# Optimization experiments

Measured on AMD Instinct MI355X. Metric: run time of the kernel, lower is better.

The kernel has to match this reference:

```python
import jax, jax.numpy as jnp
import numpy as np

N_NODES = 50000
N_EDGES = 800000
N_GRAPHS = 64
F_IN = 128
HID = 64
HEADS = 4
N_CLS = 10
NEG_SLOPE = 0.2


def _glorot(key, shape):
    fan_in, fan_out = shape[-1], shape[-2] if len(shape) > 1 else shape[-1]
    lim = jnp.sqrt(6.0 / (fan_in + fan_out))
    return jax.random.uniform(key, shape, jnp.float32, -lim, lim)


def setup_inputs() -> dict:
    key = jax.random.key(0)
    ks = jax.random.split(key, 20)
    x = jax.random.normal(ks[0], (N_NODES, F_IN), jnp.float32)
    edge_index = jax.random.randint(ks[1], (2, N_EDGES), 0, N_NODES, jnp.int32)
    batch = jnp.sort(jax.random.randint(ks[2], (N_NODES,), 0, N_GRAPHS, jnp.int32))
    HC = HID * HEADS
    return {
        "x": x, "edge_index": edge_index, "batch": batch,
        # node embedding Linear(F_IN -> HID)
        "W_emb": _glorot(ks[3], (HID, F_IN)), "b_emb": jnp.zeros((HID,), jnp.float32),
        # gat1: HID -> HID, heads=4, concat
        "W1": _glorot(ks[4], (HC, HID)),
        "a_src1": _glorot(ks[5], (HEADS, HID)), "a_dst1": _glorot(ks[6], (HEADS, HID)),
        "b1": jnp.zeros((HC,), jnp.float32),
        # gat2: HC -> HID, heads=4, concat
        "W2": _glorot(ks[7], (HC, HC)),
        "a_src2": _glorot(ks[8], (HEADS, HID)), "a_dst2": _glorot(ks[9], (HEADS, HID)),
        "b2": jnp.zeros((HC,), jnp.float32),
        # gat3: HC -> HID, heads=1, mean
        "W3": _glorot(ks[10], (HID, HC)),
        "a_src3": _glorot(ks[11], (1, HID)), "a_dst3": _glorot(ks[12], (1, HID)),
        "b3": jnp.zeros((HID,), jnp.float32),
        # classifier: Linear(2*HID -> HID), ReLU, Linear(HID -> N_CLS)
        "Wc1": _glorot(ks[13], (HID, 2 * HID)), "bc1": jnp.zeros((HID,), jnp.float32),
        "Wc2": _glorot(ks[14], (N_CLS, HID)), "bc2": jnp.zeros((N_CLS,), jnp.float32),
    }


def _gat_layer(x, src, dst, W, a_src, a_dst, b, concat):
    """PyG-style GATConv (eval mode, self-loops already in src/dst)."""
    N = x.shape[0]
    H, C = a_src.shape
    h = (x @ W.T).reshape(N, H, C)                       # [N,H,C]
    s = jnp.einsum("nhc,hc->nh", h, a_src)               # [N,H]
    d = jnp.einsum("nhc,hc->nh", h, a_dst)               # [N,H]
    e = jax.nn.leaky_relu(s[src] + d[dst], NEG_SLOPE)    # [E,H]
    emax = jax.lax.stop_gradient(jax.ops.segment_max(e, dst, num_segments=N))
    emax = jnp.where(jnp.isfinite(emax), emax, 0.0)
    ex = jnp.exp(e - emax[dst])
    den = jax.ops.segment_sum(ex, dst, num_segments=N)   # [N,H]
    alpha = ex / (den[dst] + 1e-16)                      # segment softmax
    out = jax.ops.segment_sum(h[src] * alpha[:, :, None], dst, num_segments=N)
    out = out.reshape(N, H * C) if concat else out.mean(axis=1)
    return out + b


def reference(x, edge_index, batch, W_emb, b_emb, W1, a_src1, a_dst1, b1,
              W2, a_src2, a_dst2, b2, W3, a_src3, a_dst3, b3, Wc1, bc1, Wc2, bc2):
    N = x.shape[0]
    loops = jnp.arange(N, dtype=edge_index.dtype)
    src = jnp.concatenate([edge_index[0], loops])
    dst = jnp.concatenate([edge_index[1], loops])

    h = x @ W_emb.T + b_emb
    h = jax.nn.elu(_gat_layer(h, src, dst, W1, a_src1, a_dst1, b1, True))
    h = jax.nn.elu(_gat_layer(h, src, dst, W2, a_src2, a_dst2, b2, True))
    h = jax.nn.elu(_gat_layer(h, src, dst, W3, a_src3, a_dst3, b3, False))

    counts = jax.ops.segment_sum(jnp.ones((N,), h.dtype), batch, num_segments=N_GRAPHS)
    mean = jax.ops.segment_sum(h, batch, num_segments=N_GRAPHS) / jnp.maximum(counts, 1.0)[:, None]
    mx = jax.ops.segment_max(h, batch, num_segments=N_GRAPHS)
    mx = jnp.where(counts[:, None] > 0, mx, 0.0)
    g = jnp.concatenate([mean, mx], axis=1)              # [B, 2*HID]

    g = jax.nn.relu(g @ Wc1.T + bc1)
    return g @ Wc2.T + bc2                               # [B, N_CLS]
```

## Files before the change

kernel.cpp:

```cpp
#include <hip/hip_runtime.h>
#include <math.h>

#define NG 64
#define F_IN 128
#define NEG_SLOPE 0.2f

typedef __attribute__((ext_vector_type(8))) short s16x8;
typedef __attribute__((ext_vector_type(4))) float f32x4;

static __device__ __forceinline__ float elu_f(float x) { return x > 0.f ? x : expm1f(x); }
static __device__ __forceinline__ float lrelu(float x) { return x > 0.f ? x : NEG_SLOPE * x; }
static __device__ __forceinline__ unsigned enc_f32(float x) {
    unsigned u = __float_as_uint(x);
    return (u & 0x80000000u) ? ~u : (u | 0x80000000u);
}
static __device__ __forceinline__ float dec_f32(unsigned u) {
    unsigned b = (u & 0x80000000u) ? (u & 0x7fffffffu) : ~u;
    return __uint_as_float(b);
}
static __device__ __forceinline__ unsigned short bf16_rn(float x) {
    unsigned u = __float_as_uint(x);
    unsigned r = u + 0x7FFFu + ((u >> 16) & 1u);
    return (unsigned short)(r >> 16);
}
static __device__ __forceinline__ float bf16_to_f32(unsigned short h) {
    return __uint_as_float(((unsigned)h) << 16);
}
static __device__ __forceinline__ unsigned pack_split(float x) {
    unsigned short hi = bf16_rn(x);
    unsigned short lo = bf16_rn(x - bf16_to_f32(hi));
    return ((unsigned)hi << 16) | lo;
}

__global__ void convert_pack(const float* __restrict__ in, unsigned* __restrict__ out, int n) {
    int idx = (blockIdx.x * blockDim.x + threadIdx.x) * 4;
    if (idx + 3 < n) {
        float4 v = *(const float4*)&in[idx];
        uint4 o;
        o.x = pack_split(v.x); o.y = pack_split(v.y);
        o.z = pack_split(v.z); o.w = pack_split(v.w);
        *(uint4*)&out[idx] = o;
    }
}

__global__ void uvec_kernel(const float* __restrict__ W1, const float* __restrict__ a1s,
                            const float* __restrict__ a1d,
                            float* __restrict__ us, float* __restrict__ ud) {
    int h = threadIdx.x >> 6;
    int i = threadIdx.x & 63;
    float s = 0.f, d = 0.f;
    for (int o = 0; o < 64; ++o) {
        float w = W1[(h * 64 + o) * 64 + i];
        s = fmaf(w, a1s[h * 64 + o], s);
        d = fmaf(w, a1d[h * 64 + o], d);
    }
    us[h * 64 + i] = s;
    ud[h * 64 + i] = d;
}

__global__ void hist_kernel(const int* __restrict__ ei, int* __restrict__ cnt, int E, int N) {
    int e = blockIdx.x * blockDim.x + threadIdx.x;
    int ET = E + N;
    if (e >= ET) return;
    int dst = (e < E) ? ei[E + e] : (e - E);
    atomicAdd(&cnt[dst], 1);
}

__global__ void scan1_kernel(const int* __restrict__ cnt, int* __restrict__ excl,
                             int* __restrict__ bsum, int n) {
    __shared__ int sm[256];
    int t = threadIdx.x;
    int base = blockIdx.x * 1024 + t * 4;
    int v[4];
    #pragma unroll
    for (int u = 0; u < 4; ++u) { int idx = base + u; v[u] = (idx < n) ? cnt[idx] : 0; }
    int tsum = v[0] + v[1] + v[2] + v[3];
    sm[t] = tsum;
    __syncthreads();
    for (int off = 1; off < 256; off <<= 1) {
        int y = (t >= off) ? sm[t - off] : 0;
        __syncthreads();
        sm[t] += y;
        __syncthreads();
    }
    int run = sm[t] - tsum;
    #pragma unroll
    for (int u = 0; u < 4; ++u) {
        int idx = base + u;
        if (idx < n) excl[idx] = run;
        run += v[u];
    }
    if (t == 255) bsum[blockIdx.x] = sm[255];
}

__global__ void scan2_kernel(int* __restrict__ bsum, int* __restrict__ offs, int nb, int n) {
    if (blockIdx.x == 0 && threadIdx.x == 0) {
        int run = 0;
        for (int b = 0; b < nb; ++b) { int t = bsum[b]; bsum[b] = run; run += t; }
        offs[n] = run;
    }
}

__global__ void scan3_kernel(int* __restrict__ offs, const int* __restrict__ bsum, int n) {
    int base = blockIdx.x * 1024 + threadIdx.x * 4;
    int add = bsum[blockIdx.x];
    #pragma unroll
    for (int u = 0; u < 4; ++u) { int idx = base + u; if (idx < n) offs[idx] += add; }
}

__global__ void scatter_kernel(const int* __restrict__ ei, const int* __restrict__ offs,
                               int* __restrict__ cursor, int* __restrict__ csr_src, int E, int N) {
    int e = blockIdx.x * blockDim.x + threadIdx.x;
    int ET = E + N;
    if (e >= ET) return;
    int src, dst;
    if (e < E) { src = ei[e]; dst = ei[E + e]; }
    else       { src = e - E; dst = e - E; }
    int pos = offs[dst] + atomicAdd(&cursor[dst], 1);
    csr_src[pos] = src;
}

template<int K, int BN, int HATT, bool SHARED, bool SLICED, bool DO_ELU, bool OUT_BF16>
__global__ __launch_bounds__(256) void gemm_mfma(const float* __restrict__ A, int lda,
                                                 const unsigned* __restrict__ Wp,
                                                 void* __restrict__ OutV, int M,
                                                 const float* __restrict__ bias,
                                                 const float* __restrict__ asrc,
                                                 const float* __restrict__ adst,
                                                 float* __restrict__ S, float* __restrict__ D,
                                                 int N) {
    const int NC = BN / 16;
    __shared__ __align__(16) unsigned short As_hi[64][40];
    __shared__ __align__(16) unsigned short As_lo[64][40];
    __shared__ __align__(16) unsigned short Bs_hi[BN][40];
    __shared__ __align__(16) unsigned short Bs_lo[BN][40];

    const int t = threadIdx.x;
    const int lane = t & 63;
    const int w = t >> 6;
    const int wr0 = w * 16;
    const int n0 = blockIdx.x * 64;
    const int m0 = blockIdx.y * BN;
    const int lj = lane & 15;
    const int kg = lane >> 4;
    const int aoff = SLICED ? blockIdx.y * K : 0;
    const unsigned* __restrict__ Wb = SLICED ? (Wp + (size_t)blockIdx.y * BN * K) : Wp;

    f32x4 acc[NC];
    #pragma unroll
    for (int c = 0; c < NC; ++c) acc[c] = (f32x4){0.f, 0.f, 0.f, 0.f};

    for (int kc = 0; kc < K; kc += 32) {
        __syncthreads();
        {
            int row = t >> 2, seg = t & 3;
            int gr = n0 + row;
            float v[8];
            if (gr < N) {
                float4 v0 = *(const float4*)&A[(size_t)gr * lda + aoff + kc + seg * 8];
                float4 v1 = *(const float4*)&A[(size_t)gr * lda + aoff + kc + seg * 8 + 4];
                v[0]=v0.x; v[1]=v0.y; v[2]=v0.z; v[3]=v0.w;
                v[4]=v1.x; v[5]=v1.y; v[6]=v1.z; v[7]=v1.w;
            } else {
                #pragma unroll
                for (int u = 0; u < 8; ++u) v[u] = 0.f;
            }
            unsigned hw[4], lw[4];
            #pragma unroll
            for (int p = 0; p < 4; ++p) {
                unsigned short h0 = bf16_rn(v[2*p]),   h1 = bf16_rn(v[2*p+1]);
                unsigned short l0 = bf16_rn(v[2*p]   - bf16_to_f32(h0));
                unsigned short l1 = bf16_rn(v[2*p+1] - bf16_to_f32(h1));
                hw[p] = (unsigned)h0 | ((unsigned)h1 << 16);
                lw[p] = (unsigned)l0 | ((unsigned)l1 << 16);
            }
            *(uint4*)&As_hi[row][seg * 8] = make_uint4(hw[0], hw[1], hw[2], hw[3]);
            *(uint4*)&As_lo[row][seg * 8] = make_uint4(lw[0], lw[1], lw[2], lw[3]);
        }
        #pragma unroll
        for (int it = 0; it < BN / 64; ++it) {
            int row = (t >> 2) + it * 64, seg = t & 3;
            int wrow = SLICED ? row : (m0 + row);
            uint4 q0 = *(const uint4*)&Wb[(size_t)wrow * K + kc + seg * 8];
            uint4 q1 = *(const uint4*)&Wb[(size_t)wrow * K + kc + seg * 8 + 4];
            unsigned p[8] = {q0.x, q0.y, q0.z, q0.w, q1.x, q1.y, q1.z, q1.w};
            unsigned hw[4], lw[4];
            #pragma unroll
            for (int j = 0; j < 4; ++j) {
                hw[j] = (p[2*j] >> 16) | (p[2*j+1] & 0xffff0000u);
                lw[j] = (p[2*j] & 0xffffu) | (p[2*j+1] << 16);
            }
            *(uint4*)&Bs_hi[row][seg * 8] = make_uint4(hw[0], hw[1], hw[2], hw[3]);
            *(uint4*)&Bs_lo[row][seg * 8] = make_uint4(lw[0], lw[1], lw[2], lw[3]);
        }
        __syncthreads();

        s16x8 ah = *(const s16x8*)&As_hi[wr0 + lj][kg * 8];
        s16x8 al = *(const s16x8*)&As_lo[wr0 + lj][kg * 8];
        #pragma unroll
        for (int c = 0; c < NC; ++c) {
            s16x8 bh = *(const s16x8*)&Bs_hi[c * 16 + lj][kg * 8];
            s16x8 bl = *(const s16x8*)&Bs_lo[c * 16 + lj][kg * 8];
            acc[c] = __builtin_amdgcn_mfma_f32_16x16x32_bf16(ah, bh, acc[c], 0, 0, 0);
            acc[c] = __builtin_amdgcn_mfma_f32_16x16x32_bf16(ah, bl, acc[c], 0, 0, 0);
            acc[c] = __builtin_amdgcn_mfma_f32_16x16x32_bf16(al, bh, acc[c], 0, 0, 0);
        }
    }

    #pragma unroll
    for (int c = 0; c < NC; ++c) {
        float bv = bias ? bias[m0 + c * 16 + lj] : 0.f;
        #pragma unroll
        for (int r = 0; r < 4; ++r) {
            int gn = n0 + wr0 + (lane >> 4) * 4 + r;
            if (gn < N) {
                float o = acc[c][r] + bv;
                if (DO_ELU) o = elu_f(o);
                if (OUT_BF16)
                    ((unsigned short*)OutV)[(size_t)gn * M + m0 + c * 16 + lj] = bf16_rn(o);
                else
                    ((float*)OutV)[(size_t)gn * M + m0 + c * 16 + lj] = o;
            }
        }
    }
    if (HATT > 0) {
        #pragma unroll
        for (int hh = 0; hh < HATT; ++hh) {
            float aw[4], dw[4], bw[4];
            #pragma unroll
            for (int c2 = 0; c2 < 4; ++c2) {
                aw[c2] = asrc[hh * 64 + c2 * 16 + lj];
                dw[c2] = adst[hh * 64 + c2 * 16 + lj];
                int ci = SHARED ? c2 : hh * 4 + c2;
                bw[c2] = bias ? bias[m0 + ci * 16 + lj] : 0.f;
            }
            #pragma unroll
            for (int r = 0; r < 4; ++r) {
                float sp = 0.f, dp = 0.f;
                #pragma unroll
                for (int c2 = 0; c2 < 4; ++c2) {
                    int ci = SHARED ? c2 : hh * 4 + c2;
                    float vv = acc[ci][r] + bw[c2];
                    sp = fmaf(vv, aw[c2], sp);
                    dp = fmaf(vv, dw[c2], dp);
                }
                #pragma unroll
                for (int off = 1; off < 16; off <<= 1) {
                    sp += __shfl_xor(sp, off);
                    dp += __shfl_xor(dp, off);
                }
                if (lj == 0) {
                    int gn = n0 + wr0 + (lane >> 4) * 4 + r;
                    if (gn < N) { S[gn * HATT + hh] = sp; D[gn * HATT + hh] = dp; }
                }
            }
        }
    }
}

__global__ __launch_bounds__(256, 8) void gat_agg_x(const float* __restrict__ xA,
                                                    const float* __restrict__ s,
                                                    const float* __restrict__ d,
                                                    const int* __restrict__ offs,
                                                    const int* __restrict__ csr_src,
                                                    float* __restrict__ G,
                                                    int N) {
    __shared__ float stash[4][64 * 5];
    int wv = threadIdx.x >> 6;
    int lane = threadIdx.x & 63;
    int node = (blockIdx.x * blockDim.x + threadIdx.x) >> 6;
    if (node >= N) return;
    float* st = stash[wv];
    int e0 = offs[node], e1 = offs[node + 1];
    float4 dv4 = *(const float4*)&d[node * 4];
    float dd[4] = {dv4.x, dv4.y, dv4.z, dv4.w};
    float mrun[4] = {-INFINITY, -INFINITY, -INFINITY, -INFINITY};
    float den[4] = {0.f, 0.f, 0.f, 0.f};
    float acc[4] = {0.f, 0.f, 0.f, 0.f};

    for (int base = e0; base < e1; base += 64) {
        int cnt = min(64, e1 - base);
        float ev[4] = {-INFINITY, -INFINITY, -INFINITY, -INFINITY};
        if (lane < cnt) {
            int src = csr_src[base + lane];
            float4 sv = *(const float4*)&s[src * 4];
            ev[0] = lrelu(sv.x + dd[0]); ev[1] = lrelu(sv.y + dd[1]);
            ev[2] = lrelu(sv.z + dd[2]); ev[3] = lrelu(sv.w + dd[3]);
            st[lane * 5 + 0] = ev[0]; st[lane * 5 + 1] = ev[1];
            st[lane * 5 + 2] = ev[2]; st[lane * 5 + 3] = ev[3];
            st[lane * 5 + 4] = __int_as_float(src);
        }
        #pragma unroll
        for (int h = 0; h < 4; ++h) {
            float m = ev[h];
            #pragma unroll
            for (int off = 32; off; off >>= 1) m = fmaxf(m, __shfl_xor(m, off));
            float mnew = fmaxf(mrun[h], m);
            float scale = __expf(mrun[h] - mnew);
            acc[h] *= scale; den[h] *= scale;
            mrun[h] = mnew;
        }
        int k = 0;
        for (; k + 4 <= cnt; k += 4) {
            int si[4];
            #pragma unroll
            for (int u = 0; u < 4; ++u) si[u] = __float_as_int(st[(k + u) * 5 + 4]);
            float vx[4];
            #pragma unroll
            for (int u = 0; u < 4; ++u) vx[u] = xA[(size_t)si[u] * 64 + lane];
            #pragma unroll
            for (int u = 0; u < 4; ++u) {
                #pragma unroll
                for (int h = 0; h < 4; ++h) {
                    float p = __expf(st[(k + u) * 5 + h] - mrun[h]);
                    den[h] += p;
                    acc[h] = fmaf(p, vx[u], acc[h]);
                }
            }
        }
        for (; k < cnt; ++k) {
            int src = __float_as_int(st[k * 5 + 4]);
            float v = xA[(size_t)src * 64 + lane];
            #pragma unroll
            for (int h = 0; h < 4; ++h) {
                float p = __expf(st[k * 5 + h] - mrun[h]);
                den[h] += p;
                acc[h] = fmaf(p, v, acc[h]);
            }
        }
    }
    #pragma unroll
    for (int h = 0; h < 4; ++h)
        G[(size_t)node * 256 + h * 64 + lane] = acc[h] / (den[h] + 1e-16f);
}

template<int H, bool BF16IN>
__global__ __launch_bounds__(256, 8) void gat_agg(const void* __restrict__ hLV,
                                                  const float* __restrict__ s,
                                                  const float* __restrict__ d,
                                                  const int* __restrict__ offs,
                                                  const int* __restrict__ csr_src,
                                                  const float* __restrict__ bias,
                                                  float* __restrict__ out, int N) {
    const int SW = (H == 4) ? 5 : 2;
    __shared__ float stash[4][64 * 5];
    int wv = threadIdx.x >> 6;
    int lane = threadIdx.x & 63;
    int node = (blockIdx.x * blockDim.x + threadIdx.x) >> 6;
    if (node >= N) return;
    float* st = stash[wv];
    int e0 = offs[node], e1 = offs[node + 1];
    const float* hf = (const float*)hLV;
    const unsigned short* hp = (const unsigned short*)hLV;

    float dd[H];
    #pragma unroll
    for (int h = 0; h < H; ++h) dd[h] = d[node * H + h];

    const int hd = (H == 4) ? (lane >> 4) : 0;

    float mrun = -INFINITY;
    float acc0 = 0.f, acc1 = 0.f, acc2 = 0.f, acc3 = 0.f, den = 0.f;

    for (int base = e0; base < e1; base += 64) {
        int cnt = min(64, e1 - base);
        float ev[H];
        #pragma unroll
        for (int h = 0; h < H; ++h) ev[h] = -INFINITY;
        if (lane < cnt) {
            int src = csr_src[base + lane];
            if (H == 4) {
                float4 sv = *(const float4*)&s[src * 4];
                ev[0] = lrelu(sv.x + dd[0]); ev[1] = lrelu(sv.y + dd[1]);
                ev[2] = lrelu(sv.z + dd[2]); ev[3] = lrelu(sv.w + dd[3]);
                st[lane * 5 + 0] = ev[0]; st[lane * 5 + 1] = ev[1];
                st[lane * 5 + 2] = ev[2]; st[lane * 5 + 3] = ev[3];
                st[lane * 5 + 4] = __int_as_float(src);
            } else {
                ev[0] = lrelu(s[src] + dd[0]);
                st[lane * 2 + 0] = ev[0];
                st[lane * 2 + 1] = __int_as_float(src);
            }
        }
        float mc[H];
        #pragma unroll
        for (int h = 0; h < H; ++h) {
            float m = ev[h];
            #pragma unroll
            for (int off = 32; off; off >>= 1) m = fmaxf(m, __shfl_xor(m, off));
            mc[h] = m;
        }
        float mch = mc[0];
        if (H == 4)
            mch = (lane & 32) ? ((lane & 16) ? mc[3] : mc[2]) : ((lane & 16) ? mc[1] : mc[0]);
        float mnew = fmaxf(mrun, mch);
        float scale = __expf(mrun - mnew);
        acc0 *= scale; acc1 *= scale; acc2 *= scale; acc3 *= scale; den *= scale;
        mrun = mnew;

        int k = 0;
        for (; k + 4 <= cnt; k += 4) {
            float ea = st[(k + 0) * SW + hd];
            float eb = st[(k + 1) * SW + hd];
            float ec = st[(k + 2) * SW + hd];
            float ed = st[(k + 3) * SW + hd];
            int sa = __float_as_int(st[(k + 0) * SW + SW - 1]);
            int sb = __float_as_int(st[(k + 1) * SW + SW - 1]);
            int sc = __float_as_int(st[(k + 2) * SW + SW - 1]);
            int sd_ = __float_as_int(st[(k + 3) * SW + SW - 1]);
            float pa = __expf(ea - mrun);
            float pb = __expf(eb - mrun);
            float pc = __expf(ec - mrun);
            float pd = __expf(ed - mrun);
            den += (pa + pb) + (pc + pd);
            if (H == 4) {
                if (BF16IN) {
                    uint2 ua = *(const uint2*)&hp[(size_t)sa * 256 + lane * 4];
                    uint2 ub = *(const uint2*)&hp[(size_t)sb * 256 + lane * 4];
                    uint2 uc = *(const uint2*)&hp[(size_t)sc * 256 + lane * 4];
                    uint2 ud = *(const uint2*)&hp[(size_t)sd_ * 256 + lane * 4];
                    acc0 = fmaf(pa, __uint_as_float((ua.x & 0xffffu) << 16), acc0);
                    acc1 = fmaf(pa, __uint_as_float(ua.x & 0xffff0000u), acc1);
                    acc2 = fmaf(pa, __uint_as_float((ua.y & 0xffffu) << 16), acc2);
                    acc3 = fmaf(pa, __uint_as_float(ua.y & 0xffff0000u), acc3);
                    acc0 = fmaf(pb, __uint_as_float((ub.x & 0xffffu) << 16), acc0);
                    acc1 = fmaf(pb, __uint_as_float(ub.x & 0xffff0000u), acc1);
                    acc2 = fmaf(pb, __uint_as_float((ub.y & 0xffffu) << 16), acc2);
                    acc3 = fmaf(pb, __uint_as_float(ub.y & 0xffff0000u), acc3);
                    acc0 = fmaf(pc, __uint_as_float((uc.x & 0xffffu) << 16), acc0);
                    acc1 = fmaf(pc, __uint_as_float(uc.x & 0xffff0000u), acc1);
                    acc2 = fmaf(pc, __uint_as_float((uc.y & 0xffffu) << 16), acc2);
                    acc3 = fmaf(pc, __uint_as_float(uc.y & 0xffff0000u), acc3);
                    acc0 = fmaf(pd, __uint_as_float((ud.x & 0xffffu) << 16), acc0);
                    acc1 = fmaf(pd, __uint_as_float(ud.x & 0xffff0000u), acc1);
                    acc2 = fmaf(pd, __uint_as_float((ud.y & 0xffffu) << 16), acc2);
                    acc3 = fmaf(pd, __uint_as_float(ud.y & 0xffff0000u), acc3);
                } else {
                    float4 ha = *(const float4*)&hf[(size_t)sa * 256 + lane * 4];
                    float4 hb = *(const float4*)&hf[(size_t)sb * 256 + lane * 4];
                    float4 hc = *(const float4*)&hf[(size_t)sc * 256 + lane * 4];
                    float4 hdv = *(const float4*)&hf[(size_t)sd_ * 256 + lane * 4];
                    acc0 = fmaf(pa, ha.x, acc0); acc1 = fmaf(pa, ha.y, acc1);
                    acc2 = fmaf(pa, ha.z, acc2); acc3 = fmaf(pa, ha.w, acc3);
                    acc0 = fmaf(pb, hb.x, acc0); acc1 = fmaf(pb, hb.y, acc1);
                    acc2 = fmaf(pb, hb.z, acc2); acc3 = fmaf(pb, hb.w, acc3);
                    acc0 = fmaf(pc, hc.x, acc0); acc1 = fmaf(pc, hc.y, acc1);
                    acc2 = fmaf(pc, hc.z, acc2); acc3 = fmaf(pc, hc.w, acc3);
                    acc0 = fmaf(pd, hdv.x, acc0); acc1 = fmaf(pd, hdv.y, acc1);
                    acc2 = fmaf(pd, hdv.z, acc2); acc3 = fmaf(pd, hdv.w, acc3);
                }
            } else {
                float ha, hb, hc, hdv;
                if (BF16IN) {
                    ha = bf16_to_f32(hp[(size_t)sa * 64 + lane]);
                    hb = bf16_to_f32(hp[(size_t)sb * 64 + lane]);
                    hc = bf16_to_f32(hp[(size_t)sc * 64 + lane]);
                    hdv = bf16_to_f32(hp[(size_t)sd_ * 64 + lane]);
                } else {
                    ha = hf[(size_t)sa * 64 + lane];
                    hb = hf[(size_t)sb * 64 + lane];
                    hc = hf[(size_t)sc * 64 + lane];
                    hdv = hf[(size_t)sd_ * 64 + lane];
                }
                acc0 = fmaf(pa, ha, acc0);
                acc0 = fmaf(pb, hb, acc0);
                acc0 = fmaf(pc, hc, acc0);
                acc0 = fmaf(pd, hdv, acc0);
            }
        }
        for (; k < cnt; ++k) {
            float e = st[k * SW + hd];
            int src = __float_as_int(st[k * SW + SW - 1]);
            float p = __expf(e - mrun);
            den += p;
            if (H == 4) {
                if (BF16IN) {
                    uint2 uv = *(const uint2*)&hp[(size_t)src * 256 + lane * 4];
                    acc0 = fmaf(p, __uint_as_float((uv.x & 0xffffu) << 16), acc0);
                    acc1 = fmaf(p, __uint_as_float(uv.x & 0xffff0000u), acc1);
                    acc2 = fmaf(p, __uint_as_float((uv.y & 0xffffu) << 16), acc2);
                    acc3 = fmaf(p, __uint_as_float(uv.y & 0xffff0000u), acc3);
                } else {
                    float4 hv = *(const float4*)&hf[(size_t)src * 256 + lane * 4];
                    acc0 = fmaf(p, hv.x, acc0); acc1 = fmaf(p, hv.y, acc1);
                    acc2 = fmaf(p, hv.z, acc2); acc3 = fmaf(p, hv.w, acc3);
                }
            } else {
                float hv = BF16IN ? bf16_to_f32(hp[(size_t)src * 64 + lane])
                                  : hf[(size_t)src * 64 + lane];
                acc0 = fmaf(p, hv, acc0);
            }
        }
    }

    float inv = 1.0f / (den + 1e-16f);
    if (H == 4) {
        float4 bv = *(const float4*)&bias[lane * 4];
        float4 o;
        o.x = elu_f(acc0 * inv + bv.x); o.y = elu_f(acc1 * inv + bv.y);
        o.z = elu_f(acc2 * inv + bv.z); o.w = elu_f(acc3 * inv + bv.w);
        *(float4*)&out[(size_t)node * 256 + lane * 4] = o;
    } else {
        out[(size_t)node * 64 + lane] = elu_f(acc0 * inv + bias[lane]);
    }
}

__global__ void pool_init(float* gsum, unsigned* gmax, int* gcnt) {
    int t = blockIdx.x * blockDim.x + threadIdx.x;
    if (t < NG * 64) { gsum[t] = 0.f; gmax[t] = enc_f32(-INFINITY); }
    if (t < NG) gcnt[t] = 0;
}

__global__ void pool_reduce(const float* __restrict__ h3, const int* __restrict__ batch,
                            float* __restrict__ gsum, unsigned* __restrict__ gmax,
                            int* __restrict__ gcnt, int N, int per) {
    int w = (blockIdx.x * blockDim.x + threadIdx.x) >> 6;
    int lane = threadIdx.x & 63;
    int n0 = w * per;
    int n1 = min(N, n0 + per);
    float lsum = 0.f, lmax = -INFINITY;
    int cur = -1, cnt = 0;
    for (int n = n0; n < n1; ++n) {
        int g = batch[n];
        if (g != cur) {
            if (cur >= 0) {
                atomicAdd(&gsum[cur * 64 + lane], lsum);
                atomicMax(&gmax[cur * 64 + lane], enc_f32(lmax));
                if (lane == 0) atomicAdd(&gcnt[cur], cnt);
            }
            cur = g; lsum = 0.f; lmax = -INFINITY; cnt = 0;
        }
        float v = h3[(size_t)n * 64 + lane];
        lsum += v; lmax = fmaxf(lmax, v); cnt++;
    }
    if (cur >= 0) {
        atomicAdd(&gsum[cur * 64 + lane], lsum);
        atomicMax(&gmax[cur * 64 + lane], enc_f32(lmax));
        if (lane == 0) atomicAdd(&gcnt[cur], cnt);
    }
}

__global__ __launch_bounds__(128) void classifier(const float* __restrict__ gsum,
                                                  const unsigned* __restrict__ gmax,
                                                  const int* __restrict__ gcnt,
                                                  const float* __restrict__ Wc1,
                                                  const float* __restrict__ bc1,
                                                  const float* __restrict__ Wc2,
                                                  const float* __restrict__ bc2,
                                                  float* __restrict__ out) {
    __shared__ float gv[128];
    __shared__ float z1[64];
    int g = blockIdx.x, t = threadIdx.x;
    int cnt = gcnt[g];
    if (t < 64) {
        gv[t] = gsum[g * 64 + t] / fmaxf((float)cnt, 1.f);
    } else {
        float mx = dec_f32(gmax[g * 64 + (t - 64)]);
        gv[t] = (cnt > 0) ? mx : 0.f;
    }
    __syncthreads();
    if (t < 64) {
        float a = bc1[t];
        for (int k = 0; k < 128; ++k) a = fmaf(Wc1[t * 128 + k], gv[k], a);
        z1[t] = a > 0.f ? a : 0.f;
    }
    __syncthreads();
    if (t < 10) {
        float a = bc2[t];
        for (int k = 0; k < 64; ++k) a = fmaf(Wc2[t * 64 + k], z1[k], a);
        out[g * 10 + t] = a;
    }
}

extern "C" void kernel_launch(void* const* d_in, const int* in_sizes, int n_in,
                              void* d_out, int out_size, void* d_ws, size_t ws_size,
                              hipStream_t stream) {
    const float* x      = (const float*)d_in[0];
    const int*   ei     = (const int*)d_in[1];
    const int*   batch  = (const int*)d_in[2];
    const float* W_emb  = (const float*)d_in[3];
    const float* b_emb  = (const float*)d_in[4];
    const float* W1     = (const float*)d_in[5];
    const float* as1    = (const float*)d_in[6];
    const float* ad1    = (const float*)d_in[7];
    const float* b1     = (const float*)d_in[8];
    const float* W2     = (const float*)d_in[9];
    const float* as2    = (const float*)d_in[10];
    const float* ad2    = (const float*)d_in[11];
    const float* b2     = (const float*)d_in[12];
    const float* W3     = (const float*)d_in[13];
    const float* as3    = (const float*)d_in[14];
    const float* ad3    = (const float*)d_in[15];
    const float* b3     = (const float*)d_in[16];
    const float* Wc1    = (const float*)d_in[17];
    const float* bc1    = (const float*)d_in[18];
    const float* Wc2    = (const float*)d_in[19];
    const float* bc2    = (const float*)d_in[20];

    const int N = in_sizes[0] / F_IN;
    const int E = in_sizes[1] / 2;
    const int ET = E + N;

    size_t off = 0;
    auto alloc = [&](size_t bytes) -> void* {
        void* p = (char*)d_ws + off;
        off += (bytes + 255) & ~(size_t)255;
        return p;
    };
    float*    A       = (float*)alloc((size_t)N * 64 * 4);
    float*    X       = (float*)alloc((size_t)N * 256 * 4);
    float*    Y       = (float*)alloc((size_t)N * 256 * 4);
    float*    S       = (float*)alloc((size_t)N * 4 * 4);
    float*    D       = (float*)alloc((size_t)N * 4 * 4);
    unsigned* Wp_emb  = (unsigned*)alloc(64 * 128 * 4);
    unsigned* Wp1     = (unsigned*)alloc(256 * 64 * 4);
    unsigned* Wp2     = (unsigned*)alloc(256 * 256 * 4);
    unsigned* Wp3     = (unsigned*)alloc(64 * 256 * 4);
    float*    us1     = (float*)alloc(4 * 64 * 4);
    float*    ud1     = (float*)alloc(4 * 64 * 4);
    int*      offs    = (int*)alloc((size_t)(N + 1) * 4);
    int*      cnt     = (int*)alloc((size_t)N * 4);
    int*      bsum    = (int*)alloc(64 * 4);
    int*      csr_src = (int*)alloc((size_t)ET * 4);
    float*    gsum    = (float*)alloc(NG * 64 * 4);
    unsigned* gmax    = (unsigned*)alloc(NG * 64 * 4);
    int*      gcnt    = (int*)alloc(NG * 4);
    (void)ws_size; (void)n_in; (void)out_size;

    const int SCB = (N + 1023) / 1024;

    convert_pack<<<8, 256, 0, stream>>>(W_emb, Wp_emb, 64 * 128);
    convert_pack<<<16, 256, 0, stream>>>(W1, Wp1, 256 * 64);
    convert_pack<<<64, 256, 0, stream>>>(W2, Wp2, 256 * 256);
    convert_pack<<<16, 256, 0, stream>>>(W3, Wp3, 64 * 256);
    uvec_kernel<<<1, 256, 0, stream>>>(W1, as1, ad1, us1, ud1);

    hipMemsetAsync(cnt, 0, (size_t)N * 4, stream);
    hist_kernel<<<(ET + 255) / 256, 256, 0, stream>>>(ei, cnt, E, N);
    scan1_kernel<<<SCB, 256, 0, stream>>>(cnt, offs, bsum, N);
    scan2_kernel<<<1, 64, 0, stream>>>(bsum, offs, SCB, N);
    scan3_kernel<<<SCB, 256, 0, stream>>>(offs, bsum, N);
    hipMemsetAsync(cnt, 0, (size_t)N * 4, stream);
    scatter_kernel<<<(ET + 255) / 256, 256, 0, stream>>>(ei, offs, cnt, csr_src, E, N);

    const int NWV = (N * 64 + 255) / 256;
    const int GB = (N + 63) / 64;

    gemm_mfma<128, 64, 4, true, false, false, false><<<dim3(GB, 1), 256, 0, stream>>>(
        x, 128, Wp_emb, A, 64, b_emb, us1, ud1, S, D, N);
    gat_agg_x<<<NWV, 256, 0, stream>>>(A, S, D, offs, csr_src, X, N);
    gemm_mfma<64, 64, 0, false, true, true, false><<<dim3(GB, 4), 256, 0, stream>>>(
        X, 256, Wp1, Y, 256, b1, nullptr, nullptr, nullptr, nullptr, N);
    gemm_mfma<256, 256, 4, false, false, false, true><<<dim3(GB, 1), 256, 0, stream>>>(
        Y, 256, Wp2, X, 256, nullptr, as2, ad2, S, D, N);
    gat_agg<4, true><<<NWV, 256, 0, stream>>>(X, S, D, offs, csr_src, b2, Y, N);
    gemm_mfma<256, 64, 1, true, false, false, true><<<dim3(GB, 1), 256, 0, stream>>>(
        Y, 256, Wp3, A, 64, nullptr, as3, ad3, S, D, N);
    gat_agg<1, true><<<NWV, 256, 0, stream>>>(A, S, D, offs, csr_src, b3, X, N);

    pool_init<<<16, 256, 0, stream>>>(gsum, gmax, gcnt);
    int per = (N + 255) / 256;
    pool_reduce<<<64, 256, 0, stream>>>(X, batch, gsum, gmax, gcnt, N, per);
    classifier<<<NG, 128, 0, stream>>>(gsum, gmax, gcnt, Wc1, bc1, Wc2, bc2, (float*)d_out);
}
```

Before: 564.4 us.

## Drop LDS staging in MFMA GEMMs, pre-split activations and weights into bf16 hi/lo

Replaces the LDS-staged GEMM with a kernel that loads MFMA fragments directly from global memory. Producers now write activations already packed as bf16 hi/lo pairs, and weights are pre-split into separate hi and lo arrays, so the GEMM no longer converts data or synchronises the block. The 256-wide GEMM gives each wave a 64-row by 64-column tile. This removes LDS traffic and barriers but adds uncoalesced global fragment loads, wider packed intermediates, and an extra conversion pass over x.

```diff
diff --git a/kernel.cpp b/kernel.cpp
--- a/kernel.cpp
+++ b/kernel.cpp
@@ -40,6 +40,21 @@
         o.x = pack_split(v.x); o.y = pack_split(v.y);
         o.z = pack_split(v.z); o.w = pack_split(v.w);
         *(uint4*)&out[idx] = o;
+    }
+}
+
+__global__ void convert_dual(const float* __restrict__ in, unsigned short* __restrict__ hi,
+                             unsigned short* __restrict__ lo, int n) {
+    int idx = (blockIdx.x * blockDim.x + threadIdx.x) * 4;
+    if (idx + 3 < n) {
+        float4 v = *(const float4*)&in[idx];
+        ushort4 h, l;
+        h.x = bf16_rn(v.x); l.x = bf16_rn(v.x - bf16_to_f32(h.x));
+        h.y = bf16_rn(v.y); l.y = bf16_rn(v.y - bf16_to_f32(h.y));
+        h.z = bf16_rn(v.z); l.z = bf16_rn(v.z - bf16_to_f32(h.z));
+        h.w = bf16_rn(v.w); l.w = bf16_rn(v.w - bf16_to_f32(h.w));
+        *(ushort4*)&hi[idx] = h;
+        *(ushort4*)&lo[idx] = l;
     }
 }
 
@@ -120,138 +135,150 @@
     csr_src[pos] = src;
 }
 
-template<int K, int BN, int HATT, bool SHARED, bool SLICED, bool DO_ELU, bool OUT_BF16>
-__global__ __launch_bounds__(256) void gemm_mfma(const float* __restrict__ A, int lda,
-                                                 const unsigned* __restrict__ Wp,
-                                                 void* __restrict__ OutV, int M,
-                                                 const float* __restrict__ bias,
-                                                 const float* __restrict__ asrc,
-                                                 const float* __restrict__ adst,
-                                                 float* __restrict__ S, float* __restrict__ D,
-                                                 int N) {
-    const int NC = BN / 16;
-    __shared__ __align__(16) unsigned short As_hi[64][40];
-    __shared__ __align__(16) unsigned short As_lo[64][40];
-    __shared__ __align__(16) unsigned short Bs_hi[BN][40];
-    __shared__ __align__(16) unsigned short Bs_lo[BN][40];
-
+template<int K, int BN, int HATT, bool SHARED, bool SLICED, bool DO_ELU, int OUTM>
+__global__ __launch_bounds__(256) void gemm_nolds(const unsigned* __restrict__ Ap, int lda,
+                                                  const unsigned short* __restrict__ Whi,
+                                                  const unsigned short* __restrict__ Wlo,
+                                                  void* __restrict__ OutV, int M,
+                                                  const float* __restrict__ bias,
+                                                  const float* __restrict__ asrc,
+                                                  const float* __restrict__ adst,
+                                                  float* __restrict__ S, float* __restrict__ D,
+                                                  int N) {
+    constexpr int RF = (BN == 256) ? 4 : 1;
+    constexpr int CF = 4;
     const int t = threadIdx.x;
     const int lane = t & 63;
     const int w = t >> 6;
-    const int wr0 = w * 16;
+    const int lj = lane & 15;
+    const int kg = lane >> 4;
     const int n0 = blockIdx.x * 64;
     const int m0 = blockIdx.y * BN;
-    const int lj = lane & 15;
-    const int kg = lane >> 4;
+    const int rbase = (BN == 256) ? 0 : w * 16;
+    const int cbase = (BN == 256) ? w * 64 : 0;
     const int aoff = SLICED ? blockIdx.y * K : 0;
-    const unsigned* __restrict__ Wb = SLICED ? (Wp + (size_t)blockIdx.y * BN * K) : Wp;
-
-    f32x4 acc[NC];
+    const unsigned short* __restrict__ WhiB = SLICED ? Whi + (size_t)blockIdx.y * BN * K : Whi;
+    const unsigned short* __restrict__ WloB = SLICED ? Wlo + (size_t)blockIdx.y * BN * K : Wlo;
+
+    f32x4 acc[RF][CF];
     #pragma unroll
-    for (int c = 0; c < NC; ++c) acc[c] = (f32x4){0.f, 0.f, 0.f, 0.f};
+    for (int rf = 0; rf < RF; ++rf)
+        #pragma unroll
+        for (int cf = 0; cf < CF; ++cf) acc[rf][cf] = (f32x4){0.f, 0.f, 0.f, 0.f};
 
     for (int kc = 0; kc < K; kc += 32) {
-        __syncthreads();
-        {
-            int row = t >> 2, seg = t & 3;
-            int gr = n0 + row;
-            float v[8];
-            if (gr < N) {
-                float4 v0 = *(const float4*)&A[(size_t)gr * lda + aoff + kc + seg * 8];
-                float4 v1 = *(const float4*)&A[(size_t)gr * lda + aoff + kc + seg * 8 + 4];
-                v[0]=v0.x; v[1]=v0.y; v[2]=v0.z; v[3]=v0.w;
-                v[4]=v1.x; v[5]=v1.y; v[6]=v1.z; v[7]=v1.w;
+        s16x8 ah[RF], al[RF];
+        #pragma unroll
+        for (int rf = 0; rf < RF; ++rf) {
+            int row = n0 + rbase + rf * 16 + lj;
+            unsigned p[8];
+            if (row < N) {
+                uint4 q0 = *(const uint4*)&Ap[(size_t)row * lda + aoff + kc + kg * 8];
+                uint4 q1 = *(const uint4*)&Ap[(size_t)row * lda + aoff + kc + kg * 8 + 4];
+                p[0] = q0.x; p[1] = q0.y; p[2] = q0.z; p[3] = q0.w;
+                p[4] = q1.x; p[5] = q1.y; p[6] = q1.z; p[7] = q1.w;
             } else {
                 #pragma unroll
-                for (int u = 0; u < 8; ++u) v[u] = 0.f;
-            }
-            unsigned hw[4], lw[4];
-            #pragma unroll
-            for (int p = 0; p < 4; ++p) {
-                unsigned short h0 = bf16_rn(v[2*p]),   h1 = bf16_rn(v[2*p+1]);
-                unsigned short l0 = bf16_rn(v[2*p]   - bf16_to_f32(h0));
-                unsigned short l1 = bf16_rn(v[2*p+1] - bf16_to_f32(h1));
-                hw[p] = (unsigned)h0 | ((unsigned)h1 << 16);
-                lw[p] = (unsigned)l0 | ((unsigned)l1 << 16);
-            }
-            *(uint4*)&As_hi[row][seg * 8] = make_uint4(hw[0], hw[1], hw[2], hw[3]);
-            *(uint4*)&As_lo[row][seg * 8] = make_uint4(lw[0], lw[1], lw[2], lw[3]);
+                for (int i = 0; i < 8; ++i) p[i] = 0;
+            }
+            #pragma unroll
+            for (int i = 0; i < 8; ++i) {
+                ah[rf][i] = (short)(p[i] >> 16);
+                al[rf][i] = (short)(p[i] & 0xffffu);
+            }
         }
         #pragma unroll
-        for (int it = 0; it < BN / 64; ++it) {
-            int row = (t >> 2) + it * 64, seg = t & 3;
-            int wrow = SLICED ? row : (m0 + row);
-            uint4 q0 = *(const uint4*)&Wb[(size_t)wrow * K + kc + seg * 8];
-            uint4 q1 = *(const uint4*)&Wb[(size_t)wrow * K + kc + seg * 8 + 4];
-            unsigned p[8] = {q0.x, q0.y, q0.z, q0.w, q1.x, q1.y, q1.z, q1.w};
-            unsigned hw[4], lw[4];
-            #pragma unroll
-            for (int j = 0; j < 4; ++j) {
-                hw[j] = (p[2*j] >> 16) | (p[2*j+1] & 0xffff0000u);
-                lw[j] = (p[2*j] & 0xffffu) | (p[2*j+1] << 16);
-            }
-            *(uint4*)&Bs_hi[row][seg * 8] = make_uint4(hw[0], hw[1], hw[2], hw[3]);
-            *(uint4*)&Bs_lo[row][seg * 8] = make_uint4(lw[0], lw[1], lw[2], lw[3]);
-        }
-        __syncthreads();
-
-        s16x8 ah = *(const s16x8*)&As_hi[wr0 + lj][kg * 8];
-        s16x8 al = *(const s16x8*)&As_lo[wr0 + lj][kg * 8];
+        for (int cf = 0; cf < CF; ++cf) {
+            int wcol = (SLICED ? 0 : m0) + cbase + cf * 16 + lj;
+            s16x8 bh = *(const s16x8*)&WhiB[(size_t)wcol * K + kc + kg * 8];
+            s16x8 bl = *(const s16x8*)&WloB[(size_t)wcol * K + kc + kg * 8];
+            #pragma unroll
+            for (int rf = 0; rf < RF; ++rf) {
+                acc[rf][cf] = __builtin_amdgcn_mfma_f32_16x16x32_bf16(ah[rf], bh, acc[rf][cf], 0, 0, 0);
+                acc[rf][cf] = __builtin_amdgcn_mfma_f32_16x16x32_bf16(ah[rf], bl, acc[rf][cf], 0, 0, 0);
+                acc[rf][cf] = __builtin_amdgcn_mfma_f32_16x16x32_bf16(al[rf], bh, acc[rf][cf], 0, 0, 0);
+            }
+        }
+    }
+
+    #pragma unroll
+    for (int cf = 0; cf < CF; ++cf) {
+        int gcol = m0 + cbase + cf * 16 + lj;
+        float bv = bias ? bias[gcol] : 0.f;
         #pragma unroll
-        for (int c = 0; c < NC; ++c) {
-            s16x8 bh = *(const s16x8*)&Bs_hi[c * 16 + lj][kg * 8];
-            s16x8 bl = *(const s16x8*)&Bs_lo[c * 16 + lj][kg * 8];
-            acc[c] = __builtin_amdgcn_mfma_f32_16x16x32_bf16(ah, bh, acc[c], 0, 0, 0);
-            acc[c] = __builtin_amdgcn_mfma_f32_16x16x32_bf16(ah, bl, acc[c], 0, 0, 0);
-            acc[c] = __builtin_amdgcn_mfma_f32_16x16x32_bf16(al, bh, acc[c], 0, 0, 0);
-        }
-    }
-
-    #pragma unroll
-    for (int c = 0; c < NC; ++c) {
-        float bv = bias ? bias[m0 + c * 16 + lj] : 0.f;
-        #pragma unroll
-        for (int r = 0; r < 4; ++r) {
-            int gn = n0 + wr0 + (lane >> 4) * 4 + r;
-            if (gn < N) {
-                float o = acc[c][r] + bv;
-                if (DO_ELU) o = elu_f(o);
-                if (OUT_BF16)
-                    ((unsigned short*)OutV)[(size_t)gn * M + m0 + c * 16 + lj] = bf16_rn(o);
-                else
-                    ((float*)OutV)[(size_t)gn * M + m0 + c * 16 + lj] = o;
+        for (int rf = 0; rf < RF; ++rf) {
+            #pragma unroll
+            for (int r = 0; r < 4; ++r) {
+                int gn = n0 + rbase + rf * 16 + (lane >> 4) * 4 + r;
+                if (gn < N) {
+                    float o = acc[rf][cf][r] + bv;
+                    if (DO_ELU) o = elu_f(o);
+                    if (OUTM == 0)      ((float*)OutV)[(size_t)gn * M + gcol] = o;
+                    else if (OUTM == 1) ((unsigned short*)OutV)[(size_t)gn * M + gcol] = bf16_rn(o);
+                    else                ((unsigned*)OutV)[(size_t)gn * M + gcol] = pack_split(o);
+                }
             }
         }
     }
     if (HATT > 0) {
-        #pragma unroll
-        for (int hh = 0; hh < HATT; ++hh) {
-            float aw[4], dw[4], bw[4];
-            #pragma unroll
-            for (int c2 = 0; c2 < 4; ++c2) {
-                aw[c2] = asrc[hh * 64 + c2 * 16 + lj];
-                dw[c2] = adst[hh * 64 + c2 * 16 + lj];
-                int ci = SHARED ? c2 : hh * 4 + c2;
-                bw[c2] = bias ? bias[m0 + ci * 16 + lj] : 0.f;
-            }
-            #pragma unroll
-            for (int r = 0; r < 4; ++r) {
-                float sp = 0.f, dp = 0.f;
+        if (BN == 256) {
+            float aw[CF], dw[CF], bw[CF];
+            #pragma unroll
+            for (int cf = 0; cf < CF; ++cf) {
+                aw[cf] = asrc[w * 64 + cf * 16 + lj];
+                dw[cf] = adst[w * 64 + cf * 16 + lj];
+                bw[cf] = bias ? bias[m0 + cbase + cf * 16 + lj] : 0.f;
+            }
+            #pragma unroll
+            for (int rf = 0; rf < RF; ++rf) {
                 #pragma unroll
-                for (int c2 = 0; c2 < 4; ++c2) {
-                    int ci = SHARED ? c2 : hh * 4 + c2;
-                    float vv = acc[ci][r] + bw[c2];
-                    sp = fmaf(vv, aw[c2], sp);
-                    dp = fmaf(vv, dw[c2], dp);
+                for (int r = 0; r < 4; ++r) {
+                    float sp = 0.f, dp = 0.f;
+                    #pragma unroll
+                    for (int cf = 0; cf < CF; ++cf) {
+                        float vv = acc[rf][cf][r] + bw[cf];
+                        sp = fmaf(vv, aw[cf], sp);
+                        dp = fmaf(vv, dw[cf], dp);
+                    }
+                    #pragma unroll
+                    for (int off = 1; off < 16; off <<= 1) {
+                        sp += __shfl_xor(sp, off);
+                        dp += __shfl_xor(dp, off);
+                    }
+                    if (lj == 0) {
+                        int gn = n0 + rf * 16 + (lane >> 4) * 4 + r;
+                        if (gn < N) { S[gn * HATT + w] = sp; D[gn * HATT + w] = dp; }
+                    }
+                }
+            }
+        } else {
+            #pragma unroll
+            for (int hh = 0; hh < HATT; ++hh) {
+                float aw[CF], dw[CF], bw[CF];
+                #pragma unroll
+                for (int c2 = 0; c2 < CF; ++c2) {
+                    aw[c2] = asrc[hh * 64 + c2 * 16 + lj];
+                    dw[c2] = adst[hh * 64 + c2 * 16 + lj];
+                    bw[c2] = bias ? bias[m0 + c2 * 16 + lj] : 0.f;
                 }
                 #pragma unroll
-                for (int off = 1; off < 16; off <<= 1) {
-                    sp += __shfl_xor(sp, off);
-                    dp += __shfl_xor(dp, off);
-                }
-                if (lj == 0) {
-                    int gn = n0 + wr0 + (lane >> 4) * 4 + r;
-                    if (gn < N) { S[gn * HATT + hh] = sp; D[gn * HATT + hh] = dp; }
+                for (int r = 0; r < 4; ++r) {
+                    float sp = 0.f, dp = 0.f;
+                    #pragma unroll
+                    for (int c2 = 0; c2 < CF; ++c2) {
+                        float vv = acc[0][c2][r] + bw[c2];
+                        sp = fmaf(vv, aw[c2], sp);
+                        dp = fmaf(vv, dw[c2], dp);
+                    }
+                    #pragma unroll
+                    for (int off = 1; off < 16; off <<= 1) {
+                        sp += __shfl_xor(sp, off);
+                        dp += __shfl_xor(dp, off);
+                    }
+                    if (lj == 0) {
+                        int gn = n0 + w * 16 + (lane >> 4) * 4 + r;
+                        if (gn < N) { S[gn * HATT + hh] = sp; D[gn * HATT + hh] = dp; }
+                    }
                 }
             }
         }
@@ -263,7 +290,7 @@
                                                     const float* __restrict__ d,
                                                     const int* __restrict__ offs,
                                                     const int* __restrict__ csr_src,
-                                                    float* __restrict__ G,
+                                                    unsigned* __restrict__ G,
                                                     int N) {
     __shared__ float stash[4][64 * 5];
     int wv = threadIdx.x >> 6;
@@ -331,17 +358,17 @@
     }
     #pragma unroll
     for (int h = 0; h < 4; ++h)
-        G[(size_t)node * 256 + h * 64 + lane] = acc[h] / (den[h] + 1e-16f);
-}
-
-template<int H, bool BF16IN>
-__global__ __launch_bounds__(256, 8) void gat_agg(const void* __restrict__ hLV,
+        G[(size_t)node * 256 + h * 64 + lane] = pack_split(acc[h] / (den[h] + 1e-16f));
+}
+
+template<int H, bool OUTPACK>
+__global__ __launch_bounds__(256, 8) void gat_agg(const unsigned short* __restrict__ hp,
                                                   const float* __restrict__ s,
                                                   const float* __restrict__ d,
                                                   const int* __restrict__ offs,
                                                   const int* __restrict__ csr_src,
                                                   const float* __restrict__ bias,
-                                                  float* __restrict__ out, int N) {
+                                                  void* __restrict__ outV, int N) {
     const int SW = (H == 4) ? 5 : 2;
     __shared__ float stash[4][64 * 5];
     int wv = threadIdx.x >> 6;
@@ -350,8 +377,6 @@
     if (node >= N) return;
     float* st = stash[wv];
     int e0 = offs[node], e1 = offs[node + 1];
-    const float* hf = (const float*)hLV;
-    const unsigned short* hp = (const unsigned short*)hLV;
 
     float dd[H];
     #pragma unroll
@@ -414,54 +439,31 @@
             float pd = __expf(ed - mrun);
             den += (pa + pb) + (pc + pd);
             if (H == 4) {
-                if (BF16IN) {
-                    uint2 ua = *(const uint2*)&hp[(size_t)sa * 256 + lane * 4];
-                    uint2 ub = *(const uint2*)&hp[(size_t)sb * 256 + lane * 4];
-                    uint2 uc = *(const uint2*)&hp[(size_t)sc * 256 + lane * 4];
-                    uint2 ud = *(const uint2*)&hp[(size_t)sd_ * 256 + lane * 4];
-                    acc0 = fmaf(pa, __uint_as_float((ua.x & 0xffffu) << 16), acc0);
-                    acc1 = fmaf(pa, __uint_as_float(ua.x & 0xffff0000u), acc1);
-                    acc2 = fmaf(pa, __uint_as_float((ua.y & 0xffffu) << 16), acc2);
-                    acc3 = fmaf(pa, __uint_as_float(ua.y & 0xffff0000u), acc3);
-                    acc0 = fmaf(pb, __uint_as_float((ub.x & 0xffffu) << 16), acc0);
-                    acc1 = fmaf(pb, __uint_as_float(ub.x & 0xffff0000u), acc1);
-                    acc2 = fmaf(pb, __uint_as_float((ub.y & 0xffffu) << 16), acc2);
-                    acc3 = fmaf(pb, __uint_as_float(ub.y & 0xffff0000u), acc3);
-                    acc0 = fmaf(pc, __uint_as_float((uc.x & 0xffffu) << 16), acc0);
-                    acc1 = fmaf(pc, __uint_as_float(uc.x & 0xffff0000u), acc1);
-                    acc2 = fmaf(pc, __uint_as_float((uc.y & 0xffffu) << 16), acc2);
-                    acc3 = fmaf(pc, __uint_as_float(uc.y & 0xffff0000u), acc3);
-                    acc0 = fmaf(pd, __uint_as_float((ud.x & 0xffffu) << 16), acc0);
-                    acc1 = fmaf(pd, __uint_as_float(ud.x & 0xffff0000u), acc1);
-                    acc2 = fmaf(pd, __uint_as_float((ud.y & 0xffffu) << 16), acc2);
-                    acc3 = fmaf(pd, __uint_as_float(ud.y & 0xffff0000u), acc3);
-                } else {
-                    float4 ha = *(const float4*)&hf[(size_t)sa * 256 + lane * 4];
-                    float4 hb = *(const float4*)&hf[(size_t)sb * 256 + lane * 4];
-                    float4 hc = *(const float4*)&hf[(size_t)sc * 256 + lane * 4];
-                    float4 hdv = *(const float4*)&hf[(size_t)sd_ * 256 + lane * 4];
-                    acc0 = fmaf(pa, ha.x, acc0); acc1 = fmaf(pa, ha.y, acc1);
-                    acc2 = fmaf(pa, ha.z, acc2); acc3 = fmaf(pa, ha.w, acc3);
-                    acc0 = fmaf(pb, hb.x, acc0); acc1 = fmaf(pb, hb.y, acc1);
-                    acc2 = fmaf(pb, hb.z, acc2); acc3 = fmaf(pb, hb.w, acc3);
-                    acc0 = fmaf(pc, hc.x, acc0); acc1 = fmaf(pc, hc.y, acc1);
-                    acc2 = fmaf(pc, hc.z, acc2); acc3 = fmaf(pc, hc.w, acc3);
-                    acc0 = fmaf(pd, hdv.x, acc0); acc1 = fmaf(pd, hdv.y, acc1);
-                    acc2 = fmaf(pd, hdv.z, acc2); acc3 = fmaf(pd, hdv.w, acc3);
-                }
+                uint2 ua = *(const uint2*)&hp[(size_t)sa * 256 + lane * 4];
+                uint2 ub = *(const uint2*)&hp[(size_t)sb * 256 + lane * 4];
+                uint2 uc = *(const uint2*)&hp[(size_t)sc * 256 + lane * 4];
+                uint2 ud = *(const uint2*)&hp[(size_t)sd_ * 256 + lane * 4];
+                acc0 = fmaf(pa, __uint_as_float((ua.x & 0xffffu) << 16), acc0);
+                acc1 = fmaf(pa, __uint_as_float(ua.x & 0xffff0000u), acc1);
+                acc2 = fmaf(pa, __uint_as_float((ua.y & 0xffffu) << 16), acc2);
+                acc3 = fmaf(pa, __uint_as_float(ua.y & 0xffff0000u), acc3);
+                acc0 = fmaf(pb, __uint_as_float((ub.x & 0xffffu) << 16), acc0);
+                acc1 = fmaf(pb, __uint_as_float(ub.x & 0xffff0000u), acc1);
+                acc2 = fmaf(pb, __uint_as_float((ub.y & 0xffffu) << 16), acc2);
+                acc3 = fmaf(pb, __uint_as_float(ub.y & 0xffff0000u), acc3);
+                acc0 = fmaf(pc, __uint_as_float((uc.x & 0xffffu) << 16), acc0);
+                acc1 = fmaf(pc, __uint_as_float(uc.x & 0xffff0000u), acc1);
+                acc2 = fmaf(pc, __uint_as_float((uc.y & 0xffffu) << 16), acc2);
+                acc3 = fmaf(pc, __uint_as_float(uc.y & 0xffff0000u), acc3);
+                acc0 = fmaf(pd, __uint_as_float((ud.x & 0xffffu) << 16), acc0);
+                acc1 = fmaf(pd, __uint_as_float(ud.x & 0xffff0000u), acc1);
+                acc2 = fmaf(pd, __uint_as_float((ud.y & 0xffffu) << 16), acc2);
+                acc3 = fmaf(pd, __uint_as_float(ud.y & 0xffff0000u), acc3);
             } else {
-                float ha, hb, hc, hdv;
-                if (BF16IN) {
-                    ha = bf16_to_f32(hp[(size_t)sa * 64 + lane]);
-                    hb = bf16_to_f32(hp[(size_t)sb * 64 + lane]);
-                    hc = bf16_to_f32(hp[(size_t)sc * 64 + lane]);
-                    hdv = bf16_to_f32(hp[(size_t)sd_ * 64 + lane]);
-                } else {
-                    ha = hf[(size_t)sa * 64 + lane];
-                    hb = hf[(size_t)sb * 64 + lane];
-                    hc = hf[(size_t)sc * 64 + lane];
-                    hdv = hf[(size_t)sd_ * 64 + lane];
-                }
+                float ha = bf16_to_f32(hp[(size_t)sa * 64 + lane]);
+                float hb = bf16_to_f32(hp[(size_t)sb * 64 + lane]);
+                float hc = bf16_to_f32(hp[(size_t)sc * 64 + lane]);
+                float hdv = bf16_to_f32(hp[(size_t)sd_ * 64 + lane]);
                 acc0 = fmaf(pa, ha, acc0);
                 acc0 = fmaf(pb, hb, acc0);
                 acc0 = fmaf(pc, hc, acc0);
@@ -474,21 +476,13 @@
             float p = __expf(e - mrun);
             den += p;
             if (H == 4) {
-                if (BF16IN) {
-                    uint2 uv = *(const uint2*)&hp[(size_t)src * 256 + lane * 4];
-                    acc0 = fmaf(p, __uint_as_float((uv.x & 0xffffu) << 16), acc0);
-                    acc1 = fmaf(p, __uint_as_float(uv.x & 0xffff0000u), acc1);
-                    acc2 = fmaf(p, __uint_as_float((uv.y & 0xffffu) << 16), acc2);
-                    acc3 = fmaf(p, __uint_as_float(uv.y & 0xffff0000u), acc3);
-                } else {
-                    float4 hv = *(const float4*)&hf[(size_t)src * 256 + lane * 4];
-                    acc0 = fmaf(p, hv.x, acc0); acc1 = fmaf(p, hv.y, acc1);
-                    acc2 = fmaf(p, hv.z, acc2); acc3 = fmaf(p, hv.w, acc3);
-                }
+                uint2 uv = *(const uint2*)&hp[(size_t)src * 256 + lane * 4];
+                acc0 = fmaf(p, __uint_as_float((uv.x & 0xffffu) << 16), acc0);
+                acc1 = fmaf(p, __uint_as_float(uv.x & 0xffff0000u), acc1);
+                acc2 = fmaf(p, __uint_as_float((uv.y & 0xffffu) << 16), acc2);
+                acc3 = fmaf(p, __uint_as_float(uv.y & 0xffff0000u), acc3);
             } else {
-                float hv = BF16IN ? bf16_to_f32(hp[(size_t)src * 64 + lane])
-                                  : hf[(size_t)src * 64 + lane];
-                acc0 = fmaf(p, hv, acc0);
+                acc0 = fmaf(p, bf16_to_f32(hp[(size_t)src * 64 + lane]), acc0);
             }
         }
     }
@@ -496,12 +490,23 @@
     float inv = 1.0f / (den + 1e-16f);
     if (H == 4) {
         float4 bv = *(const float4*)&bias[lane * 4];
-        float4 o;
-        o.x = elu_f(acc0 * inv + bv.x); o.y = elu_f(acc1 * inv + bv.y);
-        o.z = elu_f(acc2 * inv + bv.z); o.w = elu_f(acc3 * inv + bv.w);
-        *(float4*)&out[(size_t)node * 256 + lane * 4] = o;
+        float o0 = elu_f(acc0 * inv + bv.x);
+        float o1 = elu_f(acc1 * inv + bv.y);
+        float o2 = elu_f(acc2 * inv + bv.z);
+        float o3 = elu_f(acc3 * inv + bv.w);
+        if (OUTPACK) {
+            uint4 q;
+            q.x = pack_split(o0); q.y = pack_split(o1);
+            q.z = pack_split(o2); q.w = pack_split(o3);
+            *(uint4*)&((unsigned*)outV)[(size_t)node * 256 + lane * 4] = q;
+        } else {
+            float4 o = make_float4(o0, o1, o2, o3);
+            *(float4*)&((float*)outV)[(size_t)node * 256 + lane * 4] = o;
+        }
     } else {
-        out[(size_t)node * 64 + lane] = elu_f(acc0 * inv + bias[lane]);
+        float o = elu_f(acc0 * inv + bias[lane]);
+        if (OUTPACK) ((unsigned*)outV)[(size_t)node * 64 + lane] = pack_split(o);
+        else         ((float*)outV)[(size_t)node * 64 + lane] = o;
     }
 }
 
@@ -607,15 +612,20 @@
         off += (bytes + 255) & ~(size_t)255;
         return p;
     };
-    float*    A       = (float*)alloc((size_t)N * 64 * 4);
-    float*    X       = (float*)alloc((size_t)N * 256 * 4);
-    float*    Y       = (float*)alloc((size_t)N * 256 * 4);
-    float*    S       = (float*)alloc((size_t)N * 4 * 4);
-    float*    D       = (float*)alloc((size_t)N * 4 * 4);
-    unsigned* Wp_emb  = (unsigned*)alloc(64 * 128 * 4);
-    unsigned* Wp1     = (unsigned*)alloc(256 * 64 * 4);
-    unsigned* Wp2     = (unsigned*)alloc(256 * 256 * 4);
-    unsigned* Wp3     = (unsigned*)alloc(64 * 256 * 4);
+    unsigned* X1 = (unsigned*)alloc((size_t)N * 128 * 4);
+    float*    X2 = (float*)alloc((size_t)N * 64 * 4);
+    unsigned* X3 = (unsigned*)alloc((size_t)N * 256 * 4);
+    unsigned* X4 = (unsigned*)alloc((size_t)N * 256 * 4);
+    float*    S  = (float*)alloc((size_t)N * 4 * 4);
+    float*    D  = (float*)alloc((size_t)N * 4 * 4);
+    unsigned short* WhE = (unsigned short*)alloc(64 * 128 * 2);
+    unsigned short* WlE = (unsigned short*)alloc(64 * 128 * 2);
+    unsigned short* Wh1 = (unsigned short*)alloc(256 * 64 * 2);
+    unsigned short* Wl1 = (unsigned short*)alloc(256 * 64 * 2);
+    unsigned short* Wh2 = (unsigned short*)alloc(256 * 256 * 2);
+    unsigned short* Wl2 = (unsigned short*)alloc(256 * 256 * 2);
+    unsigned short* Wh3 = (unsigned short*)alloc(64 * 256 * 2);
+    unsigned short* Wl3 = (unsigned short*)alloc(64 * 256 * 2);
     float*    us1     = (float*)alloc(4 * 64 * 4);
     float*    ud1     = (float*)alloc(4 * 64 * 4);
     int*      offs    = (int*)alloc((size_t)(N + 1) * 4);
@@ -629,10 +639,11 @@
 
     const int SCB = (N + 1023) / 1024;
 
-    convert_pack<<<8, 256, 0, stream>>>(W_emb, Wp_emb, 64 * 128);
-    convert_pack<<<16, 256, 0, stream>>>(W1, Wp1, 256 * 64);
-    convert_pack<<<64, 256, 0, stream>>>(W2, Wp2, 256 * 256);
-    convert_pack<<<16, 256, 0, stream>>>(W3, Wp3, 64 * 256);
+    convert_pack<<<(N * 128 / 4 + 255) / 256, 256, 0, stream>>>(x, X1, N * 128);
+    convert_dual<<<8, 256, 0, stream>>>(W_emb, WhE, WlE, 64 * 128);
+    convert_dual<<<16, 256, 0, stream>>>(W1, Wh1, Wl1, 256 * 64);
+    convert_dual<<<64, 256, 0, stream>>>(W2, Wh2, Wl2, 256 * 256);
+    convert_dual<<<16, 256, 0, stream>>>(W3, Wh3, Wl3, 64 * 256);
     uvec_kernel<<<1, 256, 0, stream>>>(W1, as1, ad1, us1, ud1);
 
     hipMemsetAsync(cnt, 0, (size_t)N * 4, stream);
@@ -646,20 +657,22 @@
     const int NWV = (N * 64 + 255) / 256;
     const int GB = (N + 63) / 64;
 
-    gemm_mfma<128, 64, 4, true, false, false, false><<<dim3(GB, 1), 256, 0, stream>>>(
-        x, 128, Wp_emb, A, 64, b_emb, us1, ud1, S, D, N);
-    gat_agg_x<<<NWV, 256, 0, stream>>>(A, S, D, offs, csr_src, X, N);
-    gemm_mfma<64, 64, 0, false, true, true, false><<<dim3(GB, 4), 256, 0, stream>>>(
-        X, 256, Wp1, Y, 256, b1, nullptr, nullptr, nullptr, nullptr, N);
-    gemm_mfma<256, 256, 4, false, false, false, true><<<dim3(GB, 1), 256, 0, stream>>>(
-        Y, 256, Wp2, X, 256, nullptr, as2, ad2, S, D, N);
-    gat_agg<4, true><<<NWV, 256, 0, stream>>>(X, S, D, offs, csr_src, b2, Y, N);
-    gemm_mfma<256, 64, 1, true, false, false, true><<<dim3(GB, 1), 256, 0, stream>>>(
-        Y, 256, Wp3, A, 64, nullptr, as3, ad3, S, D, N);
-    gat_agg<1, true><<<NWV, 256, 0, stream>>>(A, S, D, offs, csr_src, b3, X, N);
+    gemm_nolds<128, 64, 4, true, false, false, 0><<<dim3(GB, 1), 256, 0, stream>>>(
+        X1, 128, WhE, WlE, X2, 64, b_emb, us1, ud1, S, D, N);
+    gat_agg_x<<<NWV, 256, 0, stream>>>(X2, S, D, offs, csr_src, X3, N);
+    gemm_nolds<64, 64, 0, false, true, true, 2><<<dim3(GB, 4), 256, 0, stream>>>(
+        X3, 256, Wh1, Wl1, X4, 256, b1, nullptr, nullptr, nullptr, nullptr, N);
+    gemm_nolds<256, 256, 4, false, false, false, 1><<<dim3(GB, 1), 256, 0, stream>>>(
+        X4, 256, Wh2, Wl2, X1, 256, nullptr, as2, ad2, S, D, N);
+    gat_agg<4, true><<<NWV, 256, 0, stream>>>((const unsigned short*)X1, S, D, offs, csr_src,
+                                              b2, X3, N);
+    gemm_nolds<256, 64, 1, true, false, false, 1><<<dim3(GB, 1), 256, 0, stream>>>(
+        X3, 256, Wh3, Wl3, X2, 64, nullptr, as3, ad3, S, D, N);
+    gat_agg<1, false><<<NWV, 256, 0, stream>>>((const unsigned short*)X2, S, D, offs, csr_src,
+                                               b3, X4, N);
 
     pool_init<<<16, 256, 0, stream>>>(gsum, gmax, gcnt);
     int per = (N + 255) / 256;
-    pool_reduce<<<64, 256, 0, stream>>>(X, batch, gsum, gmax, gcnt, N, per);
+    pool_reduce<<<64, 256, 0, stream>>>((const float*)X4, batch, gsum, gmax, gcnt, N, per);
     classifier<<<NG, 128, 0, stream>>>(gsum, gmax, gcnt, Wc1, bc1, Wc2, bc2, (float*)d_out);
 }
```

Result: slower. 646.6 us (+14.6%).
